# Performance work log

Hardware: AMD Instinct MI355X
Metric: run time of the kernel (lower is better)

Reference implementation:

```python
import jax, jax.numpy as jnp
import numpy as np

TAU = 2.0      # LIF membrane time constant
VTH = 1.0      # spiking threshold (spikingjelly default)
ALPHA = 4.0    # surrogate sigmoid sharpness (spikingjelly Sigmoid default)
EPS = 1e-5     # BatchNorm eps


@jax.custom_vjp
def spike(v):
    # Heaviside(v) with surrogate sigmoid gradient
    return (v >= 0.0).astype(v.dtype)

def _spike_fwd(v):
    return spike(v), v

def _spike_bwd(v, g):
    s = jax.nn.sigmoid(ALPHA * v)
    return (g * ALPHA * s * (1.0 - s),)

spike.defvjp(_spike_fwd, _spike_bwd)


def lif(x_seq):
    # MultiStepLIFNode: x_seq [T, B, C], v_reset=0 (hard reset), detach_reset=True
    def step(v, xt):
        v = v + (xt - v) / TAU           # membrane decay + charge
        s = spike(v - VTH)               # fire
        v = v * (1.0 - jax.lax.stop_gradient(s))  # detached hard reset to 0
        return v, s
    v0 = jnp.zeros_like(x_seq[0])
    _, s_seq = jax.lax.scan(step, v0, x_seq)
    return s_seq


def block(h, w, b, gamma, beta):
    # h: [B, C_in, T] -> conv1d(k=3, pad=1) -> BN (batch stats) -> LIF -> [B, E, T]
    y = jax.lax.conv_general_dilated(h, w, window_strides=(1,), padding=[(1, 1)],
                                     dimension_numbers=('NCH', 'OIH', 'NCH'))
    y = y + b[None, :, None]
    mu = y.mean(axis=(0, 2), keepdims=True)
    var = y.var(axis=(0, 2), keepdims=True)
    y = (y - mu) * jax.lax.rsqrt(var + EPS) * gamma[None, :, None] + beta[None, :, None]
    s = lif(jnp.transpose(y, (2, 0, 1)))        # [T, B, E]
    return jnp.transpose(s, (1, 2, 0))          # [B, E, T]


def setup_inputs() -> dict:
    key = jax.random.key(0)
    ks = jax.random.split(key, 8)
    B, T, Cin, E, O = 64, 1024, 8, 256, 63
    return {
        'x':       jax.random.normal(ks[0], (B, T, Cin), jnp.float32),
        'conv0_w': jax.random.normal(ks[1], (E, Cin, 3), jnp.float32) * (1.0 / np.sqrt(Cin * 3)),
        'conv0_b': jax.random.normal(ks[2], (E,), jnp.float32) * 0.01,
        'convs_w': jax.random.normal(ks[3], (3, E, E, 3), jnp.float32) * (1.0 / np.sqrt(E * 3)),
        'convs_b': jax.random.normal(ks[4], (3, E), jnp.float32) * 0.01,
        'bn_gamma': jnp.ones((4, E), jnp.float32),
        'bn_beta':  jnp.zeros((4, E), jnp.float32),
        'head_w':  jax.random.normal(ks[5], (O, E), jnp.float32) * (1.0 / np.sqrt(E)),
        'head_b':  jnp.zeros((O,), jnp.float32),
    }


def reference(x, conv0_w, conv0_b, convs_w, convs_b, bn_gamma, bn_beta, head_w, head_b):
    h = jnp.transpose(x, (0, 2, 1))  # [B, C, T]
    h = block(h, conv0_w, conv0_b, bn_gamma[0], bn_beta[0])
    for i in range(convs_w.shape[0]):
        h = block(h, convs_w[i], convs_b[i], bn_gamma[i + 1], bn_beta[i + 1])
    h = h.mean(axis=-1)  # AdaptiveAvgPool1d(1) + squeeze -> [B, E]
    return h @ head_w.T + head_b  # [B, O]
```

## Files before the change

### kernel.cpp

```cpp
#include <hip/hip_runtime.h>
#include <hip/hip_bf16.h>
#include <stdint.h>

#define NB 64
#define NT 1024
#define CIN 8
#define NE 256
#define NO 63
#define TPAD 16
#define TROWS (NT + 2*TPAD)
#define LCH 128
#define LWU 48
#define TT 256

using bf16x8 = __attribute__((ext_vector_type(8))) short;
using f32x4  = __attribute__((ext_vector_type(4))) float;

__global__ void prep_w(const float* __restrict__ cw, __hip_bfloat16* __restrict__ wfr) {
    int F = blockIdx.x * 256 + threadIdx.x;
    int lane = F & 63;
    int x = F >> 6;
    int cph = x & 7;  x >>= 3;
    int e4  = x & 15; x >>= 4;
    int s   = x & 1;  x >>= 1;
    int k   = x % 3;
    int l   = x / 3;
    int e = e4*16 + (lane & 15);
    int cb = cph*32 + (lane >> 4)*8;
    __hip_bfloat16 outv[8];
    #pragma unroll
    for (int j = 0; j < 8; ++j) {
        float w = cw[((size_t)(l*256 + e)*256 + (cb + j))*3 + k];
        __hip_bfloat16 hi = __float2bfloat16(w);
        if (s == 0) outv[j] = hi;
        else        outv[j] = __float2bfloat16(w - __bfloat162float(hi));
    }
    *(uint4*)(wfr + (size_t)F*8) = *(uint4*)outv;
}

__global__ void conv0_kern(const float* __restrict__ x, const float* __restrict__ w0,
                           const float* __restrict__ b0, float* __restrict__ y,
                           float* __restrict__ part) {
    int b = blockIdx.y, tc = blockIdx.x;
    int e = threadIdx.x;
    int t0 = tc * 128;
    __shared__ float xs[1040];
    for (int i = threadIdx.x; i < 1040; i += 256) {
        int t = t0 - 1 + (i >> 3); int c = i & 7;
        xs[i] = (t >= 0 && t < NT) ? x[((size_t)b*NT + t)*CIN + c] : 0.0f;
    }
    __syncthreads();
    float w[24];
    #pragma unroll
    for (int j = 0; j < 24; ++j) w[j] = w0[e*24 + j];
    float bias = b0[e];
    float s = 0.0f, qq = 0.0f;
    for (int dt = 0; dt < 128; ++dt) {
        float acc = bias;
        #pragma unroll
        for (int c = 0; c < 8; ++c)
            #pragma unroll
            for (int k = 0; k < 3; ++k)
                acc += xs[(dt + k)*8 + c] * w[c*3 + k];
        y[((size_t)b*NT + t0 + dt)*NE + e] = acc;
        s += acc; qq += acc*acc;
    }
    int p = b*8 + tc;
    part[(size_t)p*512 + e]       = s;
    part[(size_t)p*512 + 256 + e] = qq;
}

__global__ void stats_final(const float* __restrict__ part, const float* __restrict__ gamma,
                            const float* __restrict__ beta, float4* __restrict__ lifp, int np) {
    int e = blockIdx.x; int lane = threadIdx.x;
    double s = 0.0, q = 0.0;
    for (int p = lane; p < np; p += 64) {
        s += (double)part[(size_t)p*512 + e];
        q += (double)part[(size_t)p*512 + 256 + e];
    }
    #pragma unroll
    for (int off = 1; off < 64; off <<= 1) {
        s += __shfl_xor(s, off, 64);
        q += __shfl_xor(q, off, 64);
    }
    if (lane == 0) {
        const double N = 65536.0;
        double mean = s / N;
        double var  = q / N - mean*mean;
        float rs = (float)(1.0 / sqrt(var + 1e-5));
        float4 o; o.x = (float)mean; o.y = rs * gamma[e]; o.z = beta[e]; o.w = 0.0f;
        lifp[e] = o;
    }
}

template<bool WS>
__global__ void lif_kern(const float* __restrict__ y, const float4* __restrict__ lifp,
                         __hip_bfloat16* __restrict__ S, float* __restrict__ pool) {
    int c = blockIdx.x, b = blockIdx.y;
    int e = threadIdx.x;
    float4 pr = lifp[e];
    float mu = pr.x, rsg = pr.y, bet = pr.z;
    const __hip_bfloat16 z   = __float2bfloat16(0.0f);
    const __hip_bfloat16 one = __float2bfloat16(1.0f);
    if (WS) {
        if (c == 0) {
            for (int r = 0; r < TPAD; ++r) S[((size_t)b*TROWS + r)*NE + e] = z;
        }
        if (c == 7) {
            for (int r = 0; r < TPAD; ++r) S[((size_t)b*TROWS + TPAD + NT + r)*NE + e] = z;
        }
    }
    int t0 = c * LCH;
    int tw = t0 - LWU; if (tw < 0) tw = 0;
    const float* yb = y + (size_t)b*NT*NE + e;
    __hip_bfloat16* sb = S + ((size_t)b*TROWS + TPAD)*NE + e;
    float v = 0.0f;
    #pragma unroll 4
    for (int t = tw; t < t0; ++t) {
        float xx = yb[(size_t)t*NE];
        float yn = (xx - mu)*rsg + bet;
        float d  = __fsub_rn(yn, v);
        v = __fadd_rn(v, __fmul_rn(d, 0.5f));
        v = (v >= 1.0f) ? 0.0f : v;
    }
    float cnt = 0.0f;
    #pragma unroll 4
    for (int t = t0; t < t0 + LCH; ++t) {
        float xx = yb[(size_t)t*NE];
        float yn = (xx - mu)*rsg + bet;
        float d  = __fsub_rn(yn, v);
        v = __fadd_rn(v, __fmul_rn(d, 0.5f));
        bool sp = (v >= 1.0f);
        if (WS) sb[(size_t)t*NE] = sp ? one : z;
        else    cnt += sp ? 1.0f : 0.0f;
        v = sp ? 0.0f : v;
    }
    if (!WS) pool[(size_t)(b*8 + c)*256 + e] = cnt;
}

#define SROWS 258

__global__ __launch_bounds__(256, 2) void conv_mfma(
    const __hip_bfloat16* __restrict__ Sp,
    const __hip_bfloat16* __restrict__ Wfr,
    const float* __restrict__ bias,
    float* __restrict__ y,
    float* __restrict__ part)
{
    __shared__ short Bbuf[SROWS*64];
    const int tid  = threadIdx.x;
    const int wave = tid >> 6, lane = tid & 63;
    const int n16  = lane & 15, q = lane >> 4;
    const int we = wave & 1, wt = wave >> 1;
    const int tt = blockIdx.x, et = blockIdx.y, b = blockIdx.z;
    const int t0 = tt * TT;

    f32x4 acc[4][8] = {};
    bf16x8 bfr[8];

    const __hip_bfloat16* Sbase = Sp + ((size_t)b*TROWS + (TPAD - 1 + t0)) * NE;

    for (int ph = 0; ph < 4; ++ph) {
        const int c0 = ph * 64;
        __syncthreads();
        for (int idx = tid; idx < SROWS*8; idx += 256) {
            int r = idx >> 3, sg = idx & 7;
            uint4 d = *(const uint4*)(Sbase + (size_t)r*NE + c0 + sg*8);
            int sgs = sg ^ (r & 7);
            *(uint4*)((char*)Bbuf + r*128 + sgs*16) = d;
        }
        __syncthreads();
        #pragma unroll 1
        for (int kk = 0; kk < 3; ++kk) {
            #pragma unroll
            for (int cc = 0; cc < 2; ++cc) {
                #pragma unroll
                for (int g = 0; g < 8; ++g) {
                    int row = wt*128 + g*16 + n16 + kk;
                    int sgs = (cc*4 + q) ^ (row & 7);
                    bfr[g] = *(const bf16x8*)((const char*)Bbuf + row*128 + sgs*16);
                }
                #pragma unroll
                for (int s = 0; s < 2; ++s) {
                    const __hip_bfloat16* wb = Wfr
                        + ((((size_t)(kk*2 + s)*16 + (et*8 + we*4))*8 + (ph*2 + cc)) << 9) + lane*8;
                    bf16x8 afr[4];
                    #pragma unroll
                    for (int f = 0; f < 4; ++f)
                        afr[f] = *(const bf16x8*)(wb + ((size_t)f << 12));
                    #pragma unroll
                    for (int f = 0; f < 4; ++f)
                        #pragma unroll
                        for (int g = 0; g < 8; ++g)
                            acc[f][g] = __builtin_amdgcn_mfma_f32_16x16x32_bf16(afr[f], bfr[g], acc[f][g], 0, 0, 0);
                }
            }
        }
    }

    float ls[16], lq[16];
    #pragma unroll
    for (int f = 0; f < 4; ++f) {
        int e_loc = et*128 + we*64 + f*16 + q*4;
        float4 bv = *(const float4*)(bias + e_loc);
        float s0=0,s1=0,s2=0,s3=0, q0=0,q1=0,q2=0,q3=0;
        #pragma unroll
        for (int g = 0; g < 8; ++g) {
            int t = t0 + wt*128 + g*16 + n16;
            f32x4 a = acc[f][g];
            float4 o;
            o.x = a[0] + bv.x; o.y = a[1] + bv.y; o.z = a[2] + bv.z; o.w = a[3] + bv.w;
            *(float4*)(y + ((size_t)b*NT + t)*NE + e_loc) = o;
            s0 += o.x; q0 += o.x*o.x;
            s1 += o.y; q1 += o.y*o.y;
            s2 += o.z; q2 += o.z*o.z;
            s3 += o.w; q3 += o.w*o.w;
        }
        ls[f*4+0]=s0; lq[f*4+0]=q0;
        ls[f*4+1]=s1; lq[f*4+1]=q1;
        ls[f*4+2]=s2; lq[f*4+2]=q2;
        ls[f*4+3]=s3; lq[f*4+3]=q3;
    }
    #pragma unroll
    for (int off = 1; off < 16; off <<= 1) {
        #pragma unroll
        for (int i = 0; i < 16; ++i) {
            ls[i] += __shfl_xor(ls[i], off, 64);
            lq[i] += __shfl_xor(lq[i], off, 64);
        }
    }
    __syncthreads();
    float* red = (float*)Bbuf;
    if (n16 == 0 && wt == 0) {
        #pragma unroll
        for (int f = 0; f < 4; ++f)
            #pragma unroll
            for (int r = 0; r < 4; ++r) {
                int el = we*64 + f*16 + q*4 + r;
                red[el] = ls[f*4+r]; red[128+el] = lq[f*4+r];
            }
    }
    __syncthreads();
    if (n16 == 0 && wt == 1) {
        #pragma unroll
        for (int f = 0; f < 4; ++f)
            #pragma unroll
            for (int r = 0; r < 4; ++r) {
                int el = we*64 + f*16 + q*4 + r;
                red[el] += ls[f*4+r]; red[128+el] += lq[f*4+r];
            }
    }
    __syncthreads();
    if (tid < 128) {
        int p = b*4 + tt;
        part[(size_t)p*512 + et*128 + tid]       = red[tid];
        part[(size_t)p*512 + 256 + et*128 + tid] = red[128 + tid];
    }
}

__global__ void head_final(const float* __restrict__ pool, const float* __restrict__ hw,
                           const float* __restrict__ hb, float* __restrict__ out) {
    int b = blockIdx.x;
    int tid = threadIdx.x;
    __shared__ float pooled[256];
    float s = 0.0f;
    #pragma unroll
    for (int c = 0; c < 8; ++c) s += pool[(size_t)(b*8 + c)*256 + tid];
    pooled[tid] = s * (1.0f/1024.0f);
    __syncthreads();
    if (tid < NO) {
        float acc = hb[tid];
        for (int c = 0; c < 256; ++c) acc += pooled[c] * hw[tid*256 + c];
        out[b*NO + tid] = acc;
    }
}

extern "C" void kernel_launch(void* const* d_in, const int* in_sizes, int n_in,
                              void* d_out, int out_size, void* d_ws, size_t ws_size,
                              hipStream_t stream) {
    (void)in_sizes; (void)n_in; (void)out_size; (void)ws_size;
    const float* x       = (const float*)d_in[0];
    const float* conv0_w = (const float*)d_in[1];
    const float* conv0_b = (const float*)d_in[2];
    const float* convs_w = (const float*)d_in[3];
    const float* convs_b = (const float*)d_in[4];
    const float* bn_g    = (const float*)d_in[5];
    const float* bn_b    = (const float*)d_in[6];
    const float* head_w  = (const float*)d_in[7];
    const float* head_b  = (const float*)d_in[8];
    float* out = (float*)d_out;

    char* ws = (char*)d_ws;
    float*          y      = (float*)ws;
    __hip_bfloat16* S      = (__hip_bfloat16*)(ws + 67108864);
    __hip_bfloat16* Wfr    = (__hip_bfloat16*)(ws + 101711872);
    float*          part   = (float*)(ws + 104071168);
    float4*         lifp   = (float4*)(ws + 105119744);
    float*          pool   = part + 131072;

    prep_w<<<576, 256, 0, stream>>>(convs_w, Wfr);
    conv0_kern<<<dim3(8, 64), 256, 0, stream>>>(x, conv0_w, conv0_b, y, part);
    stats_final<<<256, 64, 0, stream>>>(part, bn_g, bn_b, lifp, 512);
    lif_kern<true><<<dim3(8, 64), 256, 0, stream>>>(y, lifp, S, nullptr);

    for (int l = 0; l < 3; ++l) {
        conv_mfma<<<dim3(4, 2, 64), 256, 0, stream>>>(S, Wfr + (size_t)l*393216,
                                                      convs_b + l*256, y, part);
        stats_final<<<256, 64, 0, stream>>>(part, bn_g + (l+1)*256, bn_b + (l+1)*256, lifp, 256);
        if (l < 2) lif_kern<true ><<<dim3(8, 64), 256, 0, stream>>>(y, lifp, S, nullptr);
        else       lif_kern<false><<<dim3(8, 64), 256, 0, stream>>>(y, lifp, S, pool);
    }
    head_final<<<64, 256, 0, stream>>>(pool, head_w, head_b, out);
}
```

Measured before the change: 383.6 us.

## Switch spike conv GEMM to int8 MFMA with two-level quantized weights

```diff
diff --git a/kernel.cpp b/kernel.cpp
--- a/kernel.cpp
+++ b/kernel.cpp
@@ -11,31 +11,47 @@
 #define TROWS (NT + 2*TPAD)
 #define LCH 128
 #define LWU 48
-#define TT 256
-
-using bf16x8 = __attribute__((ext_vector_type(8))) short;
+
 using f32x4  = __attribute__((ext_vector_type(4))) float;
-
-__global__ void prep_w(const float* __restrict__ cw, __hip_bfloat16* __restrict__ wfr) {
-    int F = blockIdx.x * 256 + threadIdx.x;
-    int lane = F & 63;
-    int x = F >> 6;
-    int cph = x & 7;  x >>= 3;
-    int e4  = x & 15; x >>= 4;
-    int s   = x & 1;  x >>= 1;
-    int k   = x % 3;
-    int l   = x / 3;
-    int e = e4*16 + (lane & 15);
-    int cb = cph*32 + (lane >> 4)*8;
-    __hip_bfloat16 outv[8];
-    #pragma unroll
-    for (int j = 0; j < 8; ++j) {
-        float w = cw[((size_t)(l*256 + e)*256 + (cb + j))*3 + k];
-        __hip_bfloat16 hi = __float2bfloat16(w);
-        if (s == 0) outv[j] = hi;
-        else        outv[j] = __float2bfloat16(w - __bfloat162float(hi));
-    }
-    *(uint4*)(wfr + (size_t)F*8) = *(uint4*)outv;
+using i32x4  = __attribute__((ext_vector_type(4))) int;
+
+__global__ void prep_w(const float* __restrict__ cw, signed char* __restrict__ wq,
+                       float* __restrict__ sch, float* __restrict__ scl) {
+    int l = blockIdx.x >> 8, e = blockIdx.x & 255;
+    int lane = threadIdx.x;
+    float w[4][3];
+    float m = 0.0f;
+    #pragma unroll
+    for (int ci = 0; ci < 4; ++ci)
+        #pragma unroll
+        for (int k = 0; k < 3; ++k) {
+            float v = cw[((size_t)((l*256 + e)*256) + lane*4 + ci)*3 + k];
+            w[ci][k] = v; m = fmaxf(m, fabsf(v));
+        }
+    #pragma unroll
+    for (int off = 1; off < 64; off <<= 1) m = fmaxf(m, __shfl_xor(m, off, 64));
+    float sh = fmaxf(m, 1e-30f) * (1.0f/127.0f);
+    float inv = 1.0f / sh;
+    int e4 = e >> 4, n16 = e & 15;
+    #pragma unroll
+    for (int ci = 0; ci < 4; ++ci) {
+        int c = lane*4 + ci;
+        int cg = c >> 6, cr = c & 63;
+        int fl = n16 + ((cr >> 4) << 4);
+        int j = cr & 15;
+        #pragma unroll
+        for (int k = 0; k < 3; ++k) {
+            float v = w[ci][k];
+            float qh = rintf(v * inv);
+            float resid = v - qh * sh;
+            float ql = rintf(resid * inv * 256.0f);
+            ql = fminf(fmaxf(ql, -127.0f), 127.0f);
+            size_t base = ((((size_t)(l*3 + k)*2 + 0)*16 + e4)*4 + cg)*1024 + fl*16 + j;
+            wq[base]         = (signed char)(int)qh;
+            wq[base + 65536] = (signed char)(int)ql;
+        }
+    }
+    if (lane == 0) { sch[l*256 + e] = sh; scl[l*256 + e] = sh * (1.0f/256.0f); }
 }
 
 __global__ void conv0_kern(const float* __restrict__ x, const float* __restrict__ w0,
@@ -71,10 +87,10 @@
 }
 
 __global__ void stats_final(const float* __restrict__ part, const float* __restrict__ gamma,
-                            const float* __restrict__ beta, float4* __restrict__ lifp, int np) {
+                            const float* __restrict__ beta, float4* __restrict__ lifp) {
     int e = blockIdx.x; int lane = threadIdx.x;
     double s = 0.0, q = 0.0;
-    for (int p = lane; p < np; p += 64) {
+    for (int p = lane; p < 512; p += 64) {
         s += (double)part[(size_t)p*512 + e];
         q += (double)part[(size_t)p*512 + 256 + e];
     }
@@ -95,25 +111,23 @@
 
 template<bool WS>
 __global__ void lif_kern(const float* __restrict__ y, const float4* __restrict__ lifp,
-                         __hip_bfloat16* __restrict__ S, float* __restrict__ pool) {
+                         signed char* __restrict__ S, float* __restrict__ pool) {
     int c = blockIdx.x, b = blockIdx.y;
     int e = threadIdx.x;
     float4 pr = lifp[e];
     float mu = pr.x, rsg = pr.y, bet = pr.z;
-    const __hip_bfloat16 z   = __float2bfloat16(0.0f);
-    const __hip_bfloat16 one = __float2bfloat16(1.0f);
     if (WS) {
         if (c == 0) {
-            for (int r = 0; r < TPAD; ++r) S[((size_t)b*TROWS + r)*NE + e] = z;
+            for (int r = 0; r < TPAD; ++r) S[((size_t)b*TROWS + r)*NE + e] = 0;
         }
         if (c == 7) {
-            for (int r = 0; r < TPAD; ++r) S[((size_t)b*TROWS + TPAD + NT + r)*NE + e] = z;
+            for (int r = 0; r < TPAD; ++r) S[((size_t)b*TROWS + TPAD + NT + r)*NE + e] = 0;
         }
     }
     int t0 = c * LCH;
     int tw = t0 - LWU; if (tw < 0) tw = 0;
     const float* yb = y + (size_t)b*NT*NE + e;
-    __hip_bfloat16* sb = S + ((size_t)b*TROWS + TPAD)*NE + e;
+    signed char* sb = S + ((size_t)b*TROWS + TPAD)*NE + e;
     float v = 0.0f;
     #pragma unroll 4
     for (int t = tw; t < t0; ++t) {
@@ -131,85 +145,107 @@
         float d  = __fsub_rn(yn, v);
         v = __fadd_rn(v, __fmul_rn(d, 0.5f));
         bool sp = (v >= 1.0f);
-        if (WS) sb[(size_t)t*NE] = sp ? one : z;
+        if (WS) sb[(size_t)t*NE] = sp ? 1 : 0;
         else    cnt += sp ? 1.0f : 0.0f;
         v = sp ? 0.0f : v;
     }
     if (!WS) pool[(size_t)(b*8 + c)*256 + e] = cnt;
 }
 
-#define SROWS 258
-
 __global__ __launch_bounds__(256, 2) void conv_mfma(
-    const __hip_bfloat16* __restrict__ Sp,
-    const __hip_bfloat16* __restrict__ Wfr,
+    const signed char* __restrict__ Sp,
+    const signed char* __restrict__ Wq,
+    const float* __restrict__ sch, const float* __restrict__ scl,
     const float* __restrict__ bias,
     float* __restrict__ y,
     float* __restrict__ part)
 {
-    __shared__ short Bbuf[SROWS*64];
+    __shared__ signed char Bbuf[130*272];
     const int tid  = threadIdx.x;
     const int wave = tid >> 6, lane = tid & 63;
     const int n16  = lane & 15, q = lane >> 4;
     const int we = wave & 1, wt = wave >> 1;
     const int tt = blockIdx.x, et = blockIdx.y, b = blockIdx.z;
-    const int t0 = tt * TT;
-
-    f32x4 acc[4][8] = {};
-    bf16x8 bfr[8];
-
-    const __hip_bfloat16* Sbase = Sp + ((size_t)b*TROWS + (TPAD - 1 + t0)) * NE;
-
-    for (int ph = 0; ph < 4; ++ph) {
-        const int c0 = ph * 64;
-        __syncthreads();
-        for (int idx = tid; idx < SROWS*8; idx += 256) {
-            int r = idx >> 3, sg = idx & 7;
-            uint4 d = *(const uint4*)(Sbase + (size_t)r*NE + c0 + sg*8);
-            int sgs = sg ^ (r & 7);
-            *(uint4*)((char*)Bbuf + r*128 + sgs*16) = d;
-        }
-        __syncthreads();
-        #pragma unroll 1
+    const int t0 = tt * 128;
+
+    const signed char* Sbase = Sp + ((size_t)b*TROWS + (TPAD - 1 + t0)) * NE;
+    for (int idx = tid; idx < 130*16; idx += 256) {
+        int r = idx >> 4, sg = idx & 15;
+        uint4 d = *(const uint4*)(Sbase + (size_t)r*NE + sg*16);
+        *(uint4*)(Bbuf + r*272 + sg*16) = d;
+    }
+    __syncthreads();
+
+    i32x4 acch[4][4] = {};
+    #pragma unroll
+    for (int cg = 0; cg < 4; ++cg)
+        #pragma unroll
         for (int kk = 0; kk < 3; ++kk) {
-            #pragma unroll
-            for (int cc = 0; cc < 2; ++cc) {
+            i32x4 bfr[4];
+            #pragma unroll
+            for (int g = 0; g < 4; ++g) {
+                int row = wt*64 + g*16 + n16 + kk;
+                bfr[g] = *(const i32x4*)(Bbuf + row*272 + cg*64 + q*16);
+            }
+            i32x4 afr[4];
+            #pragma unroll
+            for (int f = 0; f < 4; ++f)
+                afr[f] = *(const i32x4*)(Wq + ((((size_t)(kk*2 + 0)*16 + (et*8 + we*4 + f))*4 + cg) << 10) + lane*16);
+            #pragma unroll
+            for (int f = 0; f < 4; ++f)
                 #pragma unroll
-                for (int g = 0; g < 8; ++g) {
-                    int row = wt*128 + g*16 + n16 + kk;
-                    int sgs = (cc*4 + q) ^ (row & 7);
-                    bfr[g] = *(const bf16x8*)((const char*)Bbuf + row*128 + sgs*16);
-                }
+                for (int g = 0; g < 4; ++g)
+                    acch[f][g] = __builtin_amdgcn_mfma_i32_16x16x64_i8(afr[f], bfr[g], acch[f][g], 0, 0, 0);
+        }
+    f32x4 accf[4][4];
+    #pragma unroll
+    for (int f = 0; f < 4; ++f) {
+        float4 s4 = *(const float4*)(sch + et*128 + we*64 + f*16 + q*4);
+        #pragma unroll
+        for (int g = 0; g < 4; ++g) {
+            accf[f][g][0] = (float)acch[f][g][0] * s4.x;
+            accf[f][g][1] = (float)acch[f][g][1] * s4.y;
+            accf[f][g][2] = (float)acch[f][g][2] * s4.z;
+            accf[f][g][3] = (float)acch[f][g][3] * s4.w;
+        }
+    }
+    i32x4 accl[4][4] = {};
+    #pragma unroll
+    for (int cg = 0; cg < 4; ++cg)
+        #pragma unroll
+        for (int kk = 0; kk < 3; ++kk) {
+            i32x4 bfr[4];
+            #pragma unroll
+            for (int g = 0; g < 4; ++g) {
+                int row = wt*64 + g*16 + n16 + kk;
+                bfr[g] = *(const i32x4*)(Bbuf + row*272 + cg*64 + q*16);
+            }
+            i32x4 afr[4];
+            #pragma unroll
+            for (int f = 0; f < 4; ++f)
+                afr[f] = *(const i32x4*)(Wq + ((((size_t)(kk*2 + 1)*16 + (et*8 + we*4 + f))*4 + cg) << 10) + lane*16);
+            #pragma unroll
+            for (int f = 0; f < 4; ++f)
                 #pragma unroll
-                for (int s = 0; s < 2; ++s) {
-                    const __hip_bfloat16* wb = Wfr
-                        + ((((size_t)(kk*2 + s)*16 + (et*8 + we*4))*8 + (ph*2 + cc)) << 9) + lane*8;
-                    bf16x8 afr[4];
-                    #pragma unroll
-                    for (int f = 0; f < 4; ++f)
-                        afr[f] = *(const bf16x8*)(wb + ((size_t)f << 12));
-                    #pragma unroll
-                    for (int f = 0; f < 4; ++f)
-                        #pragma unroll
-                        for (int g = 0; g < 8; ++g)
-                            acc[f][g] = __builtin_amdgcn_mfma_f32_16x16x32_bf16(afr[f], bfr[g], acc[f][g], 0, 0, 0);
-                }
-            }
-        }
-    }
+                for (int g = 0; g < 4; ++g)
+                    accl[f][g] = __builtin_amdgcn_mfma_i32_16x16x64_i8(afr[f], bfr[g], accl[f][g], 0, 0, 0);
+        }
 
     float ls[16], lq[16];
     #pragma unroll
     for (int f = 0; f < 4; ++f) {
         int e_loc = et*128 + we*64 + f*16 + q*4;
         float4 bv = *(const float4*)(bias + e_loc);
+        float4 l4 = *(const float4*)(scl + e_loc);
         float s0=0,s1=0,s2=0,s3=0, q0=0,q1=0,q2=0,q3=0;
         #pragma unroll
-        for (int g = 0; g < 8; ++g) {
-            int t = t0 + wt*128 + g*16 + n16;
-            f32x4 a = acc[f][g];
+        for (int g = 0; g < 4; ++g) {
+            int t = t0 + wt*64 + g*16 + n16;
             float4 o;
-            o.x = a[0] + bv.x; o.y = a[1] + bv.y; o.z = a[2] + bv.z; o.w = a[3] + bv.w;
+            o.x = accf[f][g][0] + l4.x*(float)accl[f][g][0] + bv.x;
+            o.y = accf[f][g][1] + l4.y*(float)accl[f][g][1] + bv.y;
+            o.z = accf[f][g][2] + l4.z*(float)accl[f][g][2] + bv.z;
+            o.w = accf[f][g][3] + l4.w*(float)accl[f][g][3] + bv.w;
             *(float4*)(y + ((size_t)b*NT + t)*NE + e_loc) = o;
             s0 += o.x; q0 += o.x*o.x;
             s1 += o.y; q1 += o.y*o.y;
@@ -252,7 +288,7 @@
     }
     __syncthreads();
     if (tid < 128) {
-        int p = b*4 + tt;
+        int p = b*8 + tt;
         part[(size_t)p*512 + et*128 + tid]       = red[tid];
         part[(size_t)p*512 + 256 + et*128 + tid] = red[128 + tid];
     }
@@ -291,22 +327,25 @@
     float* out = (float*)d_out;
 
     char* ws = (char*)d_ws;
-    float*          y      = (float*)ws;
-    __hip_bfloat16* S      = (__hip_bfloat16*)(ws + 67108864);
-    __hip_bfloat16* Wfr    = (__hip_bfloat16*)(ws + 101711872);
-    float*          part   = (float*)(ws + 104071168);
-    float4*         lifp   = (float4*)(ws + 105119744);
-    float*          pool   = part + 131072;
-
-    prep_w<<<576, 256, 0, stream>>>(convs_w, Wfr);
+    float*       y    = (float*)ws;
+    signed char* S    = (signed char*)(ws + 67108864);
+    signed char* Wq   = (signed char*)(ws + 84410368);
+    float*       sch  = (float*)(ws + 85590016);
+    float*       scl  = (float*)(ws + 85593088);
+    float*       part = (float*)(ws + 85598208);
+    float*       pool = (float*)(ws + 86646784);
+    float4*      lifp = (float4*)(ws + 87171072);
+
+    prep_w<<<768, 64, 0, stream>>>(convs_w, Wq, sch, scl);
     conv0_kern<<<dim3(8, 64), 256, 0, stream>>>(x, conv0_w, conv0_b, y, part);
-    stats_final<<<256, 64, 0, stream>>>(part, bn_g, bn_b, lifp, 512);
+    stats_final<<<256, 64, 0, stream>>>(part, bn_g, bn_b, lifp);
     lif_kern<true><<<dim3(8, 64), 256, 0, stream>>>(y, lifp, S, nullptr);
 
     for (int l = 0; l < 3; ++l) {
-        conv_mfma<<<dim3(4, 2, 64), 256, 0, stream>>>(S, Wfr + (size_t)l*393216,
+        conv_mfma<<<dim3(8, 2, 64), 256, 0, stream>>>(S, Wq + (size_t)l*393216,
+                                                      sch + l*256, scl + l*256,
                                                       convs_b + l*256, y, part);
-        stats_final<<<256, 64, 0, stream>>>(part, bn_g + (l+1)*256, bn_b + (l+1)*256, lifp, 256);
+        stats_final<<<256, 64, 0, stream>>>(part, bn_g + (l+1)*256, bn_b + (l+1)*256, lifp);
         if (l < 2) lif_kern<true ><<<dim3(8, 64), 256, 0, stream>>>(y, lifp, S, nullptr);
         else       lif_kern<false><<<dim3(8, 64), 256, 0, stream>>>(y, lifp, S, pool);
     }
```

After: 439.7 us. +14.6%, slower.

## Fuse weight prep into conv0 launch and halve conv LDS staging tile

Applied to the files above, without the earlier changes.

```diff
diff --git a/kernel.cpp b/kernel.cpp
--- a/kernel.cpp
+++ b/kernel.cpp
@@ -16,32 +16,34 @@
 using bf16x8 = __attribute__((ext_vector_type(8))) short;
 using f32x4  = __attribute__((ext_vector_type(4))) float;
 
-__global__ void prep_w(const float* __restrict__ cw, __hip_bfloat16* __restrict__ wfr) {
-    int F = blockIdx.x * 256 + threadIdx.x;
-    int lane = F & 63;
-    int x = F >> 6;
-    int cph = x & 7;  x >>= 3;
-    int e4  = x & 15; x >>= 4;
-    int s   = x & 1;  x >>= 1;
-    int k   = x % 3;
-    int l   = x / 3;
-    int e = e4*16 + (lane & 15);
-    int cb = cph*32 + (lane >> 4)*8;
-    __hip_bfloat16 outv[8];
-    #pragma unroll
-    for (int j = 0; j < 8; ++j) {
-        float w = cw[((size_t)(l*256 + e)*256 + (cb + j))*3 + k];
-        __hip_bfloat16 hi = __float2bfloat16(w);
-        if (s == 0) outv[j] = hi;
-        else        outv[j] = __float2bfloat16(w - __bfloat162float(hi));
-    }
-    *(uint4*)(wfr + (size_t)F*8) = *(uint4*)outv;
-}
-
-__global__ void conv0_kern(const float* __restrict__ x, const float* __restrict__ w0,
+__global__ void conv0_prep(const float* __restrict__ x, const float* __restrict__ w0,
                            const float* __restrict__ b0, float* __restrict__ y,
-                           float* __restrict__ part) {
-    int b = blockIdx.y, tc = blockIdx.x;
+                           float* __restrict__ part,
+                           const float* __restrict__ cw, __hip_bfloat16* __restrict__ wfr) {
+    int bid = blockIdx.x;
+    if (bid >= 512) {
+        int F = (bid - 512) * 256 + threadIdx.x;
+        int lane = F & 63;
+        int xx = F >> 6;
+        int cph = xx & 7;  xx >>= 3;
+        int e4  = xx & 15; xx >>= 4;
+        int s   = xx & 1;  xx >>= 1;
+        int k   = xx % 3;
+        int l   = xx / 3;
+        int e = e4*16 + (lane & 15);
+        int cb = cph*32 + (lane >> 4)*8;
+        __hip_bfloat16 outv[8];
+        #pragma unroll
+        for (int j = 0; j < 8; ++j) {
+            float w = cw[((size_t)(l*256 + e)*256 + (cb + j))*3 + k];
+            __hip_bfloat16 hi = __float2bfloat16(w);
+            if (s == 0) outv[j] = hi;
+            else        outv[j] = __float2bfloat16(w - __bfloat162float(hi));
+        }
+        *(uint4*)(wfr + (size_t)F*8) = *(uint4*)outv;
+        return;
+    }
+    int b = bid >> 3, tc = bid & 7;
     int e = threadIdx.x;
     int t0 = tc * 128;
     __shared__ float xs[1040];
@@ -138,8 +140,6 @@
     if (!WS) pool[(size_t)(b*8 + c)*256 + e] = cnt;
 }
 
-#define SROWS 258
-
 __global__ __launch_bounds__(256, 2) void conv_mfma(
     const __hip_bfloat16* __restrict__ Sp,
     const __hip_bfloat16* __restrict__ Wfr,
@@ -147,7 +147,7 @@
     float* __restrict__ y,
     float* __restrict__ part)
 {
-    __shared__ short Bbuf[SROWS*64];
+    __shared__ short Bbuf[260*32];
     const int tid  = threadIdx.x;
     const int wave = tid >> 6, lane = tid & 63;
     const int n16  = lane & 15, q = lane >> 4;
@@ -160,40 +160,37 @@
 
     const __hip_bfloat16* Sbase = Sp + ((size_t)b*TROWS + (TPAD - 1 + t0)) * NE;
 
-    for (int ph = 0; ph < 4; ++ph) {
-        const int c0 = ph * 64;
+    for (int ph = 0; ph < 8; ++ph) {
+        const int c0 = ph * 32;
         __syncthreads();
-        for (int idx = tid; idx < SROWS*8; idx += 256) {
-            int r = idx >> 3, sg = idx & 7;
+        for (int idx = tid; idx < 258*4; idx += 256) {
+            int r = idx >> 2, sg = idx & 3;
             uint4 d = *(const uint4*)(Sbase + (size_t)r*NE + c0 + sg*8);
-            int sgs = sg ^ (r & 7);
-            *(uint4*)((char*)Bbuf + r*128 + sgs*16) = d;
+            int sgs = sg ^ ((r >> 1) & 3);
+            *(uint4*)((char*)Bbuf + r*64 + sgs*16) = d;
         }
         __syncthreads();
         #pragma unroll 1
         for (int kk = 0; kk < 3; ++kk) {
             #pragma unroll
-            for (int cc = 0; cc < 2; ++cc) {
+            for (int g = 0; g < 8; ++g) {
+                int row = wt*128 + g*16 + n16 + kk;
+                int sgs = q ^ ((row >> 1) & 3);
+                bfr[g] = *(const bf16x8*)((const char*)Bbuf + row*64 + sgs*16);
+            }
+            #pragma unroll
+            for (int s = 0; s < 2; ++s) {
+                const __hip_bfloat16* wb = Wfr
+                    + ((((size_t)(kk*2 + s)*16 + (et*8 + we*4))*8 + ph) << 9) + lane*8;
+                bf16x8 afr[4];
                 #pragma unroll
-                for (int g = 0; g < 8; ++g) {
-                    int row = wt*128 + g*16 + n16 + kk;
-                    int sgs = (cc*4 + q) ^ (row & 7);
-                    bfr[g] = *(const bf16x8*)((const char*)Bbuf + row*128 + sgs*16);
-                }
+                for (int f = 0; f < 4; ++f)
+                    afr[f] = *(const bf16x8*)(wb + ((size_t)f << 12));
                 #pragma unroll
-                for (int s = 0; s < 2; ++s) {
-                    const __hip_bfloat16* wb = Wfr
-                        + ((((size_t)(kk*2 + s)*16 + (et*8 + we*4))*8 + (ph*2 + cc)) << 9) + lane*8;
-                    bf16x8 afr[4];
+                for (int f = 0; f < 4; ++f)
                     #pragma unroll
-                    for (int f = 0; f < 4; ++f)
-                        afr[f] = *(const bf16x8*)(wb + ((size_t)f << 12));
-                    #pragma unroll
-                    for (int f = 0; f < 4; ++f)
-                        #pragma unroll
-                        for (int g = 0; g < 8; ++g)
-                            acc[f][g] = __builtin_amdgcn_mfma_f32_16x16x32_bf16(afr[f], bfr[g], acc[f][g], 0, 0, 0);
-                }
+                    for (int g = 0; g < 8; ++g)
+                        acc[f][g] = __builtin_amdgcn_mfma_f32_16x16x32_bf16(afr[f], bfr[g], acc[f][g], 0, 0, 0);
             }
         }
     }
@@ -296,10 +293,9 @@
     __hip_bfloat16* Wfr    = (__hip_bfloat16*)(ws + 101711872);
     float*          part   = (float*)(ws + 104071168);
     float4*         lifp   = (float4*)(ws + 105119744);
-    float*          pool   = part + 131072;
-
-    prep_w<<<576, 256, 0, stream>>>(convs_w, Wfr);
-    conv0_kern<<<dim3(8, 64), 256, 0, stream>>>(x, conv0_w, conv0_b, y, part);
+    float*          pool   = (float*)(ws + 105123840);
+
+    conv0_prep<<<1088, 256, 0, stream>>>(x, conv0_w, conv0_b, y, part, convs_w, Wfr);
     stats_final<<<256, 64, 0, stream>>>(part, bn_g, bn_b, lifp, 512);
     lif_kern<true><<<dim3(8, 64), 256, 0, stream>>>(y, lifp, S, nullptr);
 
```

New measurement: 376.8 us. Within noise of the previous version (-1.8%).
